# Kernel optimization log

Hardware: AMD Instinct MI355X
Metric: run time of the kernel (lower is better)

The kernel has to match this reference:

```python
import jax, jax.numpy as jnp
import numpy as np

GRID_LON = 17  # idx = lat*17 + lon in original code


def setup_inputs() -> dict:
    key = jax.random.key(0)
    ks = jax.random.split(key, 16)
    B, S, L = 512, 256, 64
    DIM_RHO, DIM_C, HID = 256, 128, 512
    N_LAT, N_LON = 17, GRID_LON

    rho = jax.random.normal(ks[0], (B, S, DIM_RHO), dtype=jnp.float32)
    c = jax.random.normal(ks[1], (1, DIM_C, N_LAT, N_LON), dtype=jnp.float32)
    w = jax.random.uniform(ks[2], (B, S), dtype=jnp.float32, minval=1e-3, maxval=1.0)
    l = jax.random.uniform(ks[3], (B,), dtype=jnp.float32, minval=0.1, maxval=10.0)
    roads = jax.random.randint(ks[4], (B, L), 0, N_LAT * N_LON)
    lon_idx = jax.random.randint(ks[5], (B, L), 0, N_LON)
    lat_idx = jax.random.randint(ks[6], (B, L), 0, N_LAT)

    sc = lambda fan_in: 1.0 / np.sqrt(fan_in)
    # f2: MLP(128, 256, 128) with selu
    f2_W1 = jax.random.uniform(ks[7], (DIM_C, 256), jnp.float32, -sc(DIM_C), sc(DIM_C))
    f2_b1 = jnp.zeros((256,), jnp.float32)
    f2_W2 = jax.random.uniform(ks[8], (256, DIM_C), jnp.float32, -sc(256), sc(256))
    f2_b2 = jnp.zeros((DIM_C,), jnp.float32)
    # f: MLP2(dim_rho + dim_c, hidden, 1) with selu (use_selu=True)
    fin = DIM_RHO + DIM_C
    f_W1 = jax.random.uniform(ks[9], (fin, HID), jnp.float32, -sc(fin), sc(fin))
    f_b1 = jnp.zeros((HID,), jnp.float32)
    f_W21 = jax.random.uniform(ks[10], (HID, 1), jnp.float32, -sc(HID), sc(HID))
    f_b21 = jnp.zeros((1,), jnp.float32)
    f_W22 = jax.random.uniform(ks[11], (HID, 1), jnp.float32, -sc(HID), sc(HID))
    f_b22 = jnp.zeros((1,), jnp.float32)

    return dict(rho=rho, c=c, w=w, l=l, roads=roads, lon_idx=lon_idx,
                lat_idx=lat_idx, f2_W1=f2_W1, f2_b1=f2_b1, f2_W2=f2_W2,
                f2_b2=f2_b2, f_W1=f_W1, f_b1=f_b1, f_W21=f_W21, f_b21=f_b21,
                f_W22=f_W22, f_b22=f_b22)


def reference(rho, c, w, l, roads, lon_idx, lat_idx,
              f2_W1, f2_b1, f2_W2, f2_b2,
              f_W1, f_b1, f_W21, f_b21, f_W22, f_b22):
    # c: (1, dim_c, n_lat, n_lon) -> (n_lat*n_lon, dim_c)
    c3 = jnp.squeeze(c, 0)                       # (dim_c, n_lat, n_lon)
    c_flat = jnp.transpose(c3, (1, 2, 0)).reshape(-1, c3.shape[0])  # (cells, dim_c)

    # ragged gather-mean, vectorized: (B, L) cell indices -> (B, dim_c)
    idx = lat_idx * GRID_LON + lon_idx           # (B, L)
    c_traj = jnp.mean(c_flat[idx], axis=1)       # (B, dim_c)

    # f2: selu MLP (dropout inactive / eval mode)
    h = jax.nn.selu(c_traj @ f2_W1 + f2_b1)
    c_tr = h @ f2_W2 + f2_b2                     # (B, dim_c)

    # broadcast over seq and concat with rho
    S = rho.shape[1]
    c_exp = jnp.broadcast_to(c_tr[:, None, :], (rho.shape[0], S, c_tr.shape[-1]))
    x = jnp.concatenate([rho, c_exp], axis=2)    # (B, S, dim_rho + dim_c)

    # f (MLP2, selu since use_selu=True)
    h1 = jax.nn.selu(x @ f_W1 + f_b1)            # (B, S, hidden)
    logm = (h1 @ f_W21 + f_b21)[..., 0]          # (B, S)
    logv = (h1 @ f_W22 + f_b22)[..., 0]          # (B, S)

    logw = jnp.log(w)
    logm_agg = jax.nn.logsumexp(logm + logw, axis=1)       # (B,)
    logv_agg = jax.nn.logsumexp(logv + 2.0 * logw, axis=1) # (B,)
    logl = jnp.log(l)
    log_mu = logl - logm_agg
    log_lambda = logl - 3.0 * logm_agg - logv_agg
    return (log_mu, log_lambda)
```

## Files before the change

### kernel.cpp

```cpp
#include <hip/hip_runtime.h>
#include <hip/hip_bf16.h>

typedef short bf16x8 __attribute__((ext_vector_type(8)));
typedef float f32x4 __attribute__((ext_vector_type(4)));
typedef _Float16 half4 __attribute__((ext_vector_type(4)));

__device__ __forceinline__ short f2bf(float f) {
    union { float f; unsigned u; } v; v.f = f;
    unsigned r = (v.u + 0x7FFFu + ((v.u >> 16) & 1u)) >> 16;
    return (short)r;
}

__device__ __forceinline__ float selu_f(float x) {
    const float scale = 1.0507009873554805f;
    const float sa = 1.0507009873554805f * 1.6732632423543772f;
    return x > 0.f ? scale * x : sa * (__expf(x) - 1.f);
}

__global__ void __launch_bounds__(512) prep_cbias_kernel(
    const float* __restrict__ c, const int* __restrict__ lat_idx,
    const int* __restrict__ lon_idx,
    const float* __restrict__ f2W1, const float* __restrict__ f2b1,
    const float* __restrict__ f2W2, const float* __restrict__ f2b2,
    const float* __restrict__ fW1, const float* __restrict__ fb1,
    float* __restrict__ cbias)
{
    __shared__ int cells[64];
    __shared__ float ctraj[128];
    __shared__ float hbuf[256];
    __shared__ float ctrf[128];
    const int b = blockIdx.x;
    const int t = threadIdx.x;

    if (t < 64) cells[t] = lat_idx[b * 64 + t] * 17 + lon_idx[b * 64 + t];
    __syncthreads();

    if (t < 128) {
        float s = 0.f;
        #pragma unroll 8
        for (int j = 0; j < 64; ++j) s += c[t * 289 + cells[j]];
        ctraj[t] = s * (1.f / 64.f);
    }
    __syncthreads();

    if (t < 256) {
        float acc = f2b1[t];
        #pragma unroll 8
        for (int i = 0; i < 128; ++i) acc += ctraj[i] * f2W1[i * 256 + t];
        hbuf[t] = selu_f(acc);
    }
    __syncthreads();

    if (t < 128) {
        float acc = f2b2[t];
        #pragma unroll 8
        for (int i = 0; i < 256; ++i) acc += hbuf[i] * f2W2[i * 128 + t];
        ctrf[t] = acc;
    }
    __syncthreads();

    float acc = fb1[t];
    #pragma unroll 8
    for (int i = 0; i < 128; ++i) acc += ctrf[i] * fW1[(256 + i) * 512 + t];
    cbias[b * 512 + t] = acc;
}

__global__ void __launch_bounds__(256) build_w1img_kernel(
    const float* __restrict__ fW1, short* __restrict__ img)
{
    int I = blockIdx.x * 256 + threadIdx.x;
    int e = I & 7;
    int lane = (I >> 3) & 63;
    int cg = (I >> 9) & 31;
    int kc = I >> 14;
    int col = cg * 16 + (lane & 15);
    int k = kc * 32 + ((lane >> 4) << 3) + e;
    img[I] = f2bf(fW1[k * 512 + col]);
}

__global__ void __launch_bounds__(256) build_wvec_kernel(
    const float* __restrict__ fW21, const float* __restrict__ fW22,
    _Float16* __restrict__ wvec)
{
    int I = blockIdx.x * 256 + threadIdx.x;
    int e = I & 3;
    int lane = (I >> 2) & 63;
    int nc = I >> 8;
    int l15 = lane & 15, hi = lane >> 4;
    int n = nc * 16 + hi * 4 + e;
    float v = (l15 == 0) ? fW21[n] : (l15 == 1 ? fW22[n] : 0.f);
    wvec[I] = (_Float16)v;
}

__global__ void __launch_bounds__(512, 4) fused_gemm_kernel(
    const float* __restrict__ rho, const short* __restrict__ w1img,
    const float* __restrict__ cbias, const _Float16* __restrict__ wvec,
    float* __restrict__ plm, float* __restrict__ plv)
{
    __shared__ __align__(16) char smA[32768];
    __shared__ float redM[8][64];
    __shared__ float redV[8][64];

    const int tid  = threadIdx.x;
    const int lane = tid & 63;
    const int w    = tid >> 6;
    const int l15  = lane & 15;
    const int hi   = lane >> 4;

    const int b   = blockIdx.x >> 2;
    const int s0v = (blockIdx.x & 3) << 6;

    {
        const float* rbase = rho + (size_t)(b * 256 + s0v) * 256;
        #pragma unroll
        for (int i = 0; i < 4; ++i) {
            int slot = i * 512 + tid;
            int kc = slot >> 8;
            int rem = slot & 255;
            int rg = rem >> 6;
            int ls = rem & 63;
            int row = rg * 16 + (ls & 15);
            int k0 = kc * 32 + ((ls >> 4) << 3);
            const float* src = rbase + (size_t)row * 256 + k0;
            float4 f0 = *(const float4*)(src);
            float4 f1 = *(const float4*)(src + 4);
            bf16x8 h;
            h[0] = f2bf(f0.x); h[1] = f2bf(f0.y); h[2] = f2bf(f0.z); h[3] = f2bf(f0.w);
            h[4] = f2bf(f1.x); h[5] = f2bf(f1.y); h[6] = f2bf(f1.z); h[7] = f2bf(f1.w);
            *(bf16x8*)(smA + slot * 16) = h;
        }
    }
    __syncthreads();

    f32x4 acc[4][4];
    #pragma unroll
    for (int nf = 0; nf < 4; ++nf)
        #pragma unroll
        for (int sf = 0; sf < 4; ++sf)
            acc[nf][sf] = (f32x4){0.f, 0.f, 0.f, 0.f};

    const char* bp = (const char*)w1img + w * 4096 + lane * 16;

    bf16x8 bN[4];
    #pragma unroll
    for (int nf = 0; nf < 4; ++nf)
        bN[nf] = *(const bf16x8*)(bp + nf * 1024);

    #pragma unroll
    for (int kc = 0; kc < 8; ++kc) {
        bf16x8 bC[4];
        #pragma unroll
        for (int nf = 0; nf < 4; ++nf) bC[nf] = bN[nf];
        if (kc < 7) {
            #pragma unroll
            for (int nf = 0; nf < 4; ++nf)
                bN[nf] = *(const bf16x8*)(bp + (size_t)(kc + 1) * 32768 + nf * 1024);
        }
        bf16x8 aF[4];
        #pragma unroll
        for (int sf = 0; sf < 4; ++sf)
            aF[sf] = *(const bf16x8*)(smA + ((kc * 4 + sf) * 64 + lane) * 16);
        #pragma unroll
        for (int nf = 0; nf < 4; ++nf)
            #pragma unroll
            for (int sf = 0; sf < 4; ++sf)
                acc[nf][sf] = __builtin_amdgcn_mfma_f32_16x16x32_bf16(
                    bC[nf], aF[sf], acc[nf][sf], 0, 0, 0);
    }

    f32x4 rd[4];
    #pragma unroll
    for (int sf = 0; sf < 4; ++sf) rd[sf] = (f32x4){0.f, 0.f, 0.f, 0.f};

    const int wn = w * 64;
    #pragma unroll
    for (int nf = 0; nf < 4; ++nf) {
        f32x4 cbf = *(const f32x4*)(cbias + b * 512 + wn + nf * 16 + hi * 4);
        half4 wv = *(const half4*)(wvec + (size_t)(w * 4 + nf) * 256 + lane * 4);
        #pragma unroll
        for (int sf = 0; sf < 4; ++sf) {
            half4 pa;
            #pragma unroll
            for (int q = 0; q < 4; ++q)
                pa[q] = (_Float16)selu_f(acc[nf][sf][q] + cbf[q]);
            rd[sf] = __builtin_amdgcn_mfma_f32_16x16x16f16(pa, wv, rd[sf], 0, 0, 0);
        }
    }

    if (l15 == 0) {
        #pragma unroll
        for (int sf = 0; sf < 4; ++sf)
            *(f32x4*)&redM[w][sf * 16 + hi * 4] = rd[sf];
    } else if (l15 == 1) {
        #pragma unroll
        for (int sf = 0; sf < 4; ++sf)
            *(f32x4*)&redV[w][sf * 16 + hi * 4] = rd[sf];
    }

    __syncthreads();
    size_t obase = (size_t)b * 256 + s0v;
    if (tid < 64) {
        float s = 0.f;
        #pragma unroll
        for (int j = 0; j < 8; ++j) s += redM[j][tid];
        plm[obase + tid] = s;
    } else if (tid < 128) {
        int rr = tid - 64;
        float s = 0.f;
        #pragma unroll
        for (int j = 0; j < 8; ++j) s += redV[j][rr];
        plv[obase + rr] = s;
    }
}

__global__ void __launch_bounds__(64) finalize_kernel(
    const float* __restrict__ plm, const float* __restrict__ plv,
    const float* __restrict__ w, const float* __restrict__ l,
    const float* __restrict__ b21p, const float* __restrict__ b22p,
    float* __restrict__ out)
{
    const int b = blockIdx.x;
    const int lane = threadIdx.x;
    const float b21 = b21p[0], b22 = b22p[0];

    float a1[4], a2[4];
    float m1 = -1e30f, m2 = -1e30f;
    #pragma unroll
    for (int i = 0; i < 4; ++i) {
        int s = i * 64 + lane;
        float lw = logf(w[b * 256 + s]);
        a1[i] = plm[b * 256 + s] + b21 + lw;
        a2[i] = plv[b * 256 + s] + b22 + 2.f * lw;
        m1 = fmaxf(m1, a1[i]);
        m2 = fmaxf(m2, a2[i]);
    }
    #pragma unroll
    for (int m = 1; m < 64; m <<= 1) {
        m1 = fmaxf(m1, __shfl_xor(m1, m));
        m2 = fmaxf(m2, __shfl_xor(m2, m));
    }
    float s1 = 0.f, s2 = 0.f;
    #pragma unroll
    for (int i = 0; i < 4; ++i) {
        s1 += expf(a1[i] - m1);
        s2 += expf(a2[i] - m2);
    }
    #pragma unroll
    for (int m = 1; m < 64; m <<= 1) {
        s1 += __shfl_xor(s1, m);
        s2 += __shfl_xor(s2, m);
    }
    if (lane == 0) {
        float lm_agg = m1 + logf(s1);
        float lv_agg = m2 + logf(s2);
        float logl = logf(l[b]);
        out[b]       = logl - lm_agg;
        out[512 + b] = logl - 3.f * lm_agg - lv_agg;
    }
}

extern "C" void kernel_launch(void* const* d_in, const int* in_sizes, int n_in,
                              void* d_out, int out_size, void* d_ws, size_t ws_size,
                              hipStream_t stream) {
    const float* rho     = (const float*)d_in[0];
    const float* c       = (const float*)d_in[1];
    const float* w       = (const float*)d_in[2];
    const float* l       = (const float*)d_in[3];
    const int*   lon_idx = (const int*)d_in[5];
    const int*   lat_idx = (const int*)d_in[6];
    const float* f2W1    = (const float*)d_in[7];
    const float* f2b1    = (const float*)d_in[8];
    const float* f2W2    = (const float*)d_in[9];
    const float* f2b2    = (const float*)d_in[10];
    const float* fW1     = (const float*)d_in[11];
    const float* fb1     = (const float*)d_in[12];
    const float* fW21    = (const float*)d_in[13];
    const float* fb21    = (const float*)d_in[14];
    const float* fW22    = (const float*)d_in[15];
    const float* fb22    = (const float*)d_in[16];
    float* out = (float*)d_out;

    char* ws = (char*)d_ws;
    float*     cbias = (float*)(ws);
    short*     w1img = (short*)(ws + 1048576);
    float*     plm   = (float*)(ws + 1310720);
    float*     plv   = (float*)(ws + 1835008);
    _Float16*  wvec  = (_Float16*)(ws + 2359296);

    prep_cbias_kernel<<<512, 512, 0, stream>>>(c, lat_idx, lon_idx,
                                               f2W1, f2b1, f2W2, f2b2,
                                               fW1, fb1, cbias);
    build_w1img_kernel<<<512, 256, 0, stream>>>(fW1, w1img);
    build_wvec_kernel<<<32, 256, 0, stream>>>(fW21, fW22, wvec);
    fused_gemm_kernel<<<2048, 512, 0, stream>>>(rho, w1img, cbias, wvec,
                                                plm, plv);
    finalize_kernel<<<512, 64, 0, stream>>>(plm, plv, w, l, fb21, fb22, out);
}
```

Measured before the change: 98.43 us.

## Merge prep kernels and pipeline GEMM with triple-buffered LDS async loads

The three preprocessing kernels become one launch that dispatches on block index. The main GEMM moves to 1024-thread blocks covering 128 sequence rows, with a 2x8 wave grid. Weight tiles are streamed into LDS through global_load_lds, and rho chunks are converted to bf16 in a triple-buffered K loop with barriers. This aims to overlap global loads with MFMA work, cut redundant per-wave weight fetches from global memory, and save launch overhead. In exchange it uses 128KB of LDS per block, which limits occupancy, and adds two barriers per K chunk.

```diff
diff --git a/kernel.cpp b/kernel.cpp
--- a/kernel.cpp
+++ b/kernel.cpp
@@ -2,6 +2,7 @@
 #include <hip/hip_bf16.h>
 
 typedef short bf16x8 __attribute__((ext_vector_type(8)));
+typedef short bf16x4 __attribute__((ext_vector_type(4)));
 typedef float f32x4 __attribute__((ext_vector_type(4)));
 typedef _Float16 half4 __attribute__((ext_vector_type(4)));
 
@@ -17,120 +18,110 @@
     return x > 0.f ? scale * x : sa * (__expf(x) - 1.f);
 }
 
-__global__ void __launch_bounds__(512) prep_cbias_kernel(
+__device__ __forceinline__ void gld_lds16(const char* g, char* l) {
+    __builtin_amdgcn_global_load_lds(
+        (const __attribute__((address_space(1))) unsigned int*)g,
+        (__attribute__((address_space(3))) unsigned int*)l, 16, 0, 0);
+}
+
+__global__ void __launch_bounds__(512) prep_all_kernel(
     const float* __restrict__ c, const int* __restrict__ lat_idx,
     const int* __restrict__ lon_idx,
     const float* __restrict__ f2W1, const float* __restrict__ f2b1,
     const float* __restrict__ f2W2, const float* __restrict__ f2b2,
     const float* __restrict__ fW1, const float* __restrict__ fb1,
+    const float* __restrict__ fW21, const float* __restrict__ fW22,
+    short* __restrict__ w1img, _Float16* __restrict__ wvec,
     float* __restrict__ cbias)
 {
-    __shared__ int cells[64];
-    __shared__ float ctraj[128];
-    __shared__ float hbuf[256];
-    __shared__ float ctrf[128];
-    const int b = blockIdx.x;
+    const int bid = blockIdx.x;
     const int t = threadIdx.x;
 
-    if (t < 64) cells[t] = lat_idx[b * 64 + t] * 17 + lon_idx[b * 64 + t];
-    __syncthreads();
-
-    if (t < 128) {
-        float s = 0.f;
+    if (bid < 512) {
+        __shared__ int cells[64];
+        __shared__ float ctraj[128];
+        __shared__ float hbuf[256];
+        __shared__ float ctrf[128];
+        const int b = bid;
+
+        if (t < 64) cells[t] = lat_idx[b * 64 + t] * 17 + lon_idx[b * 64 + t];
+        __syncthreads();
+
+        if (t < 128) {
+            float s = 0.f;
+            #pragma unroll 8
+            for (int j = 0; j < 64; ++j) s += c[t * 289 + cells[j]];
+            ctraj[t] = s * (1.f / 64.f);
+        }
+        __syncthreads();
+
+        if (t < 256) {
+            float acc = f2b1[t];
+            #pragma unroll 8
+            for (int i = 0; i < 128; ++i) acc += ctraj[i] * f2W1[i * 256 + t];
+            hbuf[t] = selu_f(acc);
+        }
+        __syncthreads();
+
+        if (t < 128) {
+            float acc = f2b2[t];
+            #pragma unroll 8
+            for (int i = 0; i < 256; ++i) acc += hbuf[i] * f2W2[i * 128 + t];
+            ctrf[t] = acc;
+        }
+        __syncthreads();
+
+        float acc = fb1[t];
         #pragma unroll 8
-        for (int j = 0; j < 64; ++j) s += c[t * 289 + cells[j]];
-        ctraj[t] = s * (1.f / 64.f);
-    }
-    __syncthreads();
-
-    if (t < 256) {
-        float acc = f2b1[t];
-        #pragma unroll 8
-        for (int i = 0; i < 128; ++i) acc += ctraj[i] * f2W1[i * 256 + t];
-        hbuf[t] = selu_f(acc);
-    }
-    __syncthreads();
-
-    if (t < 128) {
-        float acc = f2b2[t];
-        #pragma unroll 8
-        for (int i = 0; i < 256; ++i) acc += hbuf[i] * f2W2[i * 128 + t];
-        ctrf[t] = acc;
-    }
-    __syncthreads();
-
-    float acc = fb1[t];
-    #pragma unroll 8
-    for (int i = 0; i < 128; ++i) acc += ctrf[i] * fW1[(256 + i) * 512 + t];
-    cbias[b * 512 + t] = acc;
-}
-
-__global__ void __launch_bounds__(256) build_w1img_kernel(
-    const float* __restrict__ fW1, short* __restrict__ img)
-{
-    int I = blockIdx.x * 256 + threadIdx.x;
-    int e = I & 7;
-    int lane = (I >> 3) & 63;
-    int cg = (I >> 9) & 31;
-    int kc = I >> 14;
-    int col = cg * 16 + (lane & 15);
-    int k = kc * 32 + ((lane >> 4) << 3) + e;
-    img[I] = f2bf(fW1[k * 512 + col]);
-}
-
-__global__ void __launch_bounds__(256) build_wvec_kernel(
-    const float* __restrict__ fW21, const float* __restrict__ fW22,
-    _Float16* __restrict__ wvec)
-{
-    int I = blockIdx.x * 256 + threadIdx.x;
-    int e = I & 3;
-    int lane = (I >> 2) & 63;
-    int nc = I >> 8;
-    int l15 = lane & 15, hi = lane >> 4;
-    int n = nc * 16 + hi * 4 + e;
-    float v = (l15 == 0) ? fW21[n] : (l15 == 1 ? fW22[n] : 0.f);
-    wvec[I] = (_Float16)v;
-}
-
-__global__ void __launch_bounds__(512, 4) fused_gemm_kernel(
+        for (int i = 0; i < 128; ++i) acc += ctrf[i] * fW1[(256 + i) * 512 + t];
+        cbias[b * 512 + t] = acc;
+    } else if (bid < 768) {
+        int I = (bid - 512) * 512 + t;
+        int e = I & 7;
+        int lane = (I >> 3) & 63;
+        int cg = (I >> 9) & 31;
+        int kc = I >> 14;
+        int col = cg * 16 + (lane & 15);
+        int k = kc * 32 + ((lane >> 4) << 3) + e;
+        w1img[I] = f2bf(fW1[k * 512 + col]);
+    } else {
+        int I = (bid - 768) * 512 + t;
+        int e = I & 3;
+        int lane = (I >> 2) & 63;
+        int nc = I >> 8;
+        int l15 = lane & 15, hi = lane >> 4;
+        int n = nc * 16 + hi * 4 + e;
+        float v = (l15 == 0) ? fW21[n] : (l15 == 1 ? fW22[n] : 0.f);
+        wvec[I] = (_Float16)v;
+    }
+}
+
+__global__ void __launch_bounds__(1024, 4) fused_gemm_kernel(
     const float* __restrict__ rho, const short* __restrict__ w1img,
     const float* __restrict__ cbias, const _Float16* __restrict__ wvec,
     float* __restrict__ plm, float* __restrict__ plv)
 {
-    __shared__ __align__(16) char smA[32768];
-    __shared__ float redM[8][64];
-    __shared__ float redV[8][64];
+    __shared__ __align__(16) char smem[131072];
 
     const int tid  = threadIdx.x;
     const int lane = tid & 63;
-    const int w    = tid >> 6;
+    const int wid  = tid >> 6;
+    const int wr   = wid >> 3;
+    const int wc2  = wid & 7;
     const int l15  = lane & 15;
     const int hi   = lane >> 4;
 
-    const int b   = blockIdx.x >> 2;
-    const int s0v = (blockIdx.x & 3) << 6;
-
-    {
-        const float* rbase = rho + (size_t)(b * 256 + s0v) * 256;
-        #pragma unroll
-        for (int i = 0; i < 4; ++i) {
-            int slot = i * 512 + tid;
-            int kc = slot >> 8;
-            int rem = slot & 255;
-            int rg = rem >> 6;
-            int ls = rem & 63;
-            int row = rg * 16 + (ls & 15);
-            int k0 = kc * 32 + ((ls >> 4) << 3);
-            const float* src = rbase + (size_t)row * 256 + k0;
-            float4 f0 = *(const float4*)(src);
-            float4 f1 = *(const float4*)(src + 4);
-            bf16x8 h;
-            h[0] = f2bf(f0.x); h[1] = f2bf(f0.y); h[2] = f2bf(f0.z); h[3] = f2bf(f0.w);
-            h[4] = f2bf(f1.x); h[5] = f2bf(f1.y); h[6] = f2bf(f1.z); h[7] = f2bf(f1.w);
-            *(bf16x8*)(smA + slot * 16) = h;
-        }
-    }
-    __syncthreads();
+    const int b  = blockIdx.x >> 1;
+    const int s0 = (blockIdx.x & 1) << 7;
+
+    const int rg_t = tid >> 7;
+    const int ln_t = (tid >> 1) & 63;
+    const int h_t  = tid & 1;
+    const float* prA = rho + (size_t)(b * 256 + s0 + rg_t * 16 + (ln_t & 15)) * 256
+                           + ((ln_t >> 4) << 3) + h_t * 4;
+    const int awoff = ((rg_t * 64 + ln_t) << 4) + (h_t << 3);
+
+    const char* wsrc = (const char*)w1img;
 
     f32x4 acc[4][4];
     #pragma unroll
@@ -139,44 +130,79 @@
         for (int sf = 0; sf < 4; ++sf)
             acc[nf][sf] = (f32x4){0.f, 0.f, 0.f, 0.f};
 
-    const char* bp = (const char*)w1img + w * 4096 + lane * 16;
-
-    bf16x8 bN[4];
-    #pragma unroll
-    for (int nf = 0; nf < 4; ++nf)
-        bN[nf] = *(const bf16x8*)(bp + nf * 1024);
-
-    #pragma unroll
-    for (int kc = 0; kc < 8; ++kc) {
-        bf16x8 bC[4];
-        #pragma unroll
-        for (int nf = 0; nf < 4; ++nf) bC[nf] = bN[nf];
-        if (kc < 7) {
-            #pragma unroll
-            for (int nf = 0; nf < 4; ++nf)
-                bN[nf] = *(const bf16x8*)(bp + (size_t)(kc + 1) * 32768 + nf * 1024);
-        }
-        bf16x8 aF[4];
-        #pragma unroll
-        for (int sf = 0; sf < 4; ++sf)
-            aF[sf] = *(const bf16x8*)(smA + ((kc * 4 + sf) * 64 + lane) * 16);
-        #pragma unroll
-        for (int nf = 0; nf < 4; ++nf)
-            #pragma unroll
-            for (int sf = 0; sf < 4; ++sf)
-                acc[nf][sf] = __builtin_amdgcn_mfma_f32_16x16x32_bf16(
-                    bC[nf], aF[sf], acc[nf][sf], 0, 0, 0);
-    }
+    float4 pf0, pf1;
+
+    {
+        const char* bs0 = wsrc + (wid * 2) * 1024 + lane * 16;
+        char* bd0 = smem + 24576 + (wid * 2) * 1024;
+        gld_lds16(bs0, bd0);
+        gld_lds16(bs0 + 1024, bd0 + 1024);
+        pf0 = *(const float4*)(prA);
+        const char* bs1 = wsrc + 32768 + (wid * 2) * 1024 + lane * 16;
+        char* bd1 = smem + 24576 + 32768 + (wid * 2) * 1024;
+        gld_lds16(bs1, bd1);
+        gld_lds16(bs1 + 1024, bd1 + 1024);
+        pf1 = *(const float4*)(prA + 8);
+    }
+
+#define CHUNK(I, PFX)                                                          \
+    {                                                                          \
+        {          \
+          bf16x4 hh;                                                           \
+          hh[0] = f2bf(PFX.x); hh[1] = f2bf(PFX.y);                            \
+          hh[2] = f2bf(PFX.z); hh[3] = f2bf(PFX.w);                            \
+          *(bf16x4*)(smem + ((I) % 3) * 8192 + awoff) = hh; }                  \
+        if ((I) + 2 <= 7) {    \
+            const char* bs = wsrc + ((I) + 2) * 32768 + (wid * 2) * 1024       \
+                             + lane * 16;                                      \
+            char* bd = smem + 24576 + (((I) + 2) % 3) * 32768                  \
+                       + (wid * 2) * 1024;                                     \
+            gld_lds16(bs, bd);                                                 \
+            gld_lds16(bs + 1024, bd + 1024);                                   \
+            PFX = *(const float4*)(prA + ((I) + 2) * 8);                       \
+        }                                                                      \
+        asm volatile("s_waitcnt lgkmcnt(0)" ::: "memory");                     \
+        __builtin_amdgcn_s_barrier();                                          \
+        __builtin_amdgcn_sched_barrier(0);                                     \
+        {                                                                      \
+            bf16x8 aF[4], bF[4];                                               \
+            const char* ab = smem + ((I) % 3) * 8192;                          \
+            const char* bb = smem + 24576 + ((I) % 3) * 32768;                 \
+            _Pragma("unroll")                                                  \
+            for (int sf = 0; sf < 4; ++sf)                                     \
+                aF[sf] = *(const bf16x8*)(ab + (((wr * 4 + sf) * 64 + lane) << 4)); \
+            _Pragma("unroll")                                                  \
+            for (int nf = 0; nf < 4; ++nf)                                     \
+                bF[nf] = *(const bf16x8*)(bb + (((wc2 * 4 + nf) * 64 + lane) << 4)); \
+            _Pragma("unroll")                                                  \
+            for (int nf = 0; nf < 4; ++nf)                                     \
+                _Pragma("unroll")                                              \
+                for (int sf = 0; sf < 4; ++sf)                                 \
+                    acc[nf][sf] = __builtin_amdgcn_mfma_f32_16x16x32_bf16(     \
+                        bF[nf], aF[sf], acc[nf][sf], 0, 0, 0);                 \
+        }                                                                      \
+        __builtin_amdgcn_sched_barrier(0);                                     \
+        __builtin_amdgcn_s_barrier();                                          \
+    }
+
+    CHUNK(0, pf0)
+    CHUNK(1, pf1)
+    CHUNK(2, pf0)
+    CHUNK(3, pf1)
+    CHUNK(4, pf0)
+    CHUNK(5, pf1)
+    CHUNK(6, pf0)
+    CHUNK(7, pf1)
+#undef CHUNK
 
     f32x4 rd[4];
     #pragma unroll
     for (int sf = 0; sf < 4; ++sf) rd[sf] = (f32x4){0.f, 0.f, 0.f, 0.f};
 
-    const int wn = w * 64;
     #pragma unroll
     for (int nf = 0; nf < 4; ++nf) {
-        f32x4 cbf = *(const f32x4*)(cbias + b * 512 + wn + nf * 16 + hi * 4);
-        half4 wv = *(const half4*)(wvec + (size_t)(w * 4 + nf) * 256 + lane * 4);
+        f32x4 cbf = *(const f32x4*)(cbias + b * 512 + wc2 * 64 + nf * 16 + hi * 4);
+        half4 wv = *(const half4*)(wvec + (size_t)(wc2 * 4 + nf) * 256 + lane * 4);
         #pragma unroll
         for (int sf = 0; sf < 4; ++sf) {
             half4 pa;
@@ -187,28 +213,30 @@
         }
     }
 
+    float* redM = (float*)(smem + 122880);
+    float* redV = (float*)(smem + 126976);
     if (l15 == 0) {
         #pragma unroll
         for (int sf = 0; sf < 4; ++sf)
-            *(f32x4*)&redM[w][sf * 16 + hi * 4] = rd[sf];
+            *(f32x4*)&redM[wc2 * 128 + wr * 64 + sf * 16 + hi * 4] = rd[sf];
     } else if (l15 == 1) {
         #pragma unroll
         for (int sf = 0; sf < 4; ++sf)
-            *(f32x4*)&redV[w][sf * 16 + hi * 4] = rd[sf];
+            *(f32x4*)&redV[wc2 * 128 + wr * 64 + sf * 16 + hi * 4] = rd[sf];
     }
 
     __syncthreads();
-    size_t obase = (size_t)b * 256 + s0v;
-    if (tid < 64) {
+    size_t obase = (size_t)b * 256 + s0;
+    if (tid < 128) {
         float s = 0.f;
         #pragma unroll
-        for (int j = 0; j < 8; ++j) s += redM[j][tid];
+        for (int j = 0; j < 8; ++j) s += redM[j * 128 + tid];
         plm[obase + tid] = s;
-    } else if (tid < 128) {
-        int rr = tid - 64;
+    } else if (tid < 256) {
+        int rr = tid - 128;
         float s = 0.f;
         #pragma unroll
-        for (int j = 0; j < 8; ++j) s += redV[j][rr];
+        for (int j = 0; j < 8; ++j) s += redV[j * 128 + rr];
         plv[obase + rr] = s;
     }
 }
@@ -287,12 +315,11 @@
     float*     plv   = (float*)(ws + 1835008);
     _Float16*  wvec  = (_Float16*)(ws + 2359296);
 
-    prep_cbias_kernel<<<512, 512, 0, stream>>>(c, lat_idx, lon_idx,
-                                               f2W1, f2b1, f2W2, f2b2,
-                                               fW1, fb1, cbias);
-    build_w1img_kernel<<<512, 256, 0, stream>>>(fW1, w1img);
-    build_wvec_kernel<<<32, 256, 0, stream>>>(fW21, fW22, wvec);
-    fused_gemm_kernel<<<2048, 512, 0, stream>>>(rho, w1img, cbias, wvec,
-                                                plm, plv);
+    prep_all_kernel<<<784, 512, 0, stream>>>(c, lat_idx, lon_idx,
+                                             f2W1, f2b1, f2W2, f2b2,
+                                             fW1, fb1, fW21, fW22,
+                                             w1img, wvec, cbias);
+    fused_gemm_kernel<<<1024, 1024, 0, stream>>>(rho, w1img, cbias, wvec,
+                                                 plm, plv);
     finalize_kernel<<<512, 64, 0, stream>>>(plm, plv, w, l, fb21, fb22, out);
 }
```

Result: no change. 99.94 us (+1.5%).

## Merge prep kernels and coalesce rho staging with swizzled LDS layout

Applied to the files above, without the earlier changes.

Folds the three small preparation kernels into one launch by giving each block range its own task, which removes two kernel launches and their gaps. In the GEMM kernel, rho is now read with contiguous per-thread loads and converted to bf16 with packed hardware conversion instructions. The result is stored into LDS with an XOR swizzle, and the MFMA operand reads use the matching swizzled addresses to avoid bank conflicts. The reduction buffers are carved out of the same shared allocation. The swizzle indexing must exactly match the old fragment layout, which is the main correctness risk.

```diff
diff --git a/kernel.cpp b/kernel.cpp
--- a/kernel.cpp
+++ b/kernel.cpp
@@ -17,79 +17,76 @@
     return x > 0.f ? scale * x : sa * (__expf(x) - 1.f);
 }
 
-__global__ void __launch_bounds__(512) prep_cbias_kernel(
+__global__ void __launch_bounds__(512) prep_all_kernel(
     const float* __restrict__ c, const int* __restrict__ lat_idx,
     const int* __restrict__ lon_idx,
     const float* __restrict__ f2W1, const float* __restrict__ f2b1,
     const float* __restrict__ f2W2, const float* __restrict__ f2b2,
     const float* __restrict__ fW1, const float* __restrict__ fb1,
+    const float* __restrict__ fW21, const float* __restrict__ fW22,
+    short* __restrict__ w1img, _Float16* __restrict__ wvec,
     float* __restrict__ cbias)
 {
-    __shared__ int cells[64];
-    __shared__ float ctraj[128];
-    __shared__ float hbuf[256];
-    __shared__ float ctrf[128];
-    const int b = blockIdx.x;
+    const int bid = blockIdx.x;
     const int t = threadIdx.x;
 
-    if (t < 64) cells[t] = lat_idx[b * 64 + t] * 17 + lon_idx[b * 64 + t];
-    __syncthreads();
-
-    if (t < 128) {
-        float s = 0.f;
+    if (bid < 512) {
+        __shared__ int cells[64];
+        __shared__ float ctraj[128];
+        __shared__ float hbuf[256];
+        __shared__ float ctrf[128];
+        const int b = bid;
+
+        if (t < 64) cells[t] = lat_idx[b * 64 + t] * 17 + lon_idx[b * 64 + t];
+        __syncthreads();
+
+        if (t < 128) {
+            float s = 0.f;
+            #pragma unroll 8
+            for (int j = 0; j < 64; ++j) s += c[t * 289 + cells[j]];
+            ctraj[t] = s * (1.f / 64.f);
+        }
+        __syncthreads();
+
+        if (t < 256) {
+            float acc = f2b1[t];
+            #pragma unroll 8
+            for (int i = 0; i < 128; ++i) acc += ctraj[i] * f2W1[i * 256 + t];
+            hbuf[t] = selu_f(acc);
+        }
+        __syncthreads();
+
+        if (t < 128) {
+            float acc = f2b2[t];
+            #pragma unroll 8
+            for (int i = 0; i < 256; ++i) acc += hbuf[i] * f2W2[i * 128 + t];
+            ctrf[t] = acc;
+        }
+        __syncthreads();
+
+        float acc = fb1[t];
         #pragma unroll 8
-        for (int j = 0; j < 64; ++j) s += c[t * 289 + cells[j]];
-        ctraj[t] = s * (1.f / 64.f);
-    }
-    __syncthreads();
-
-    if (t < 256) {
-        float acc = f2b1[t];
-        #pragma unroll 8
-        for (int i = 0; i < 128; ++i) acc += ctraj[i] * f2W1[i * 256 + t];
-        hbuf[t] = selu_f(acc);
-    }
-    __syncthreads();
-
-    if (t < 128) {
-        float acc = f2b2[t];
-        #pragma unroll 8
-        for (int i = 0; i < 256; ++i) acc += hbuf[i] * f2W2[i * 128 + t];
-        ctrf[t] = acc;
-    }
-    __syncthreads();
-
-    float acc = fb1[t];
-    #pragma unroll 8
-    for (int i = 0; i < 128; ++i) acc += ctrf[i] * fW1[(256 + i) * 512 + t];
-    cbias[b * 512 + t] = acc;
-}
-
-__global__ void __launch_bounds__(256) build_w1img_kernel(
-    const float* __restrict__ fW1, short* __restrict__ img)
-{
-    int I = blockIdx.x * 256 + threadIdx.x;
-    int e = I & 7;
-    int lane = (I >> 3) & 63;
-    int cg = (I >> 9) & 31;
-    int kc = I >> 14;
-    int col = cg * 16 + (lane & 15);
-    int k = kc * 32 + ((lane >> 4) << 3) + e;
-    img[I] = f2bf(fW1[k * 512 + col]);
-}
-
-__global__ void __launch_bounds__(256) build_wvec_kernel(
-    const float* __restrict__ fW21, const float* __restrict__ fW22,
-    _Float16* __restrict__ wvec)
-{
-    int I = blockIdx.x * 256 + threadIdx.x;
-    int e = I & 3;
-    int lane = (I >> 2) & 63;
-    int nc = I >> 8;
-    int l15 = lane & 15, hi = lane >> 4;
-    int n = nc * 16 + hi * 4 + e;
-    float v = (l15 == 0) ? fW21[n] : (l15 == 1 ? fW22[n] : 0.f);
-    wvec[I] = (_Float16)v;
+        for (int i = 0; i < 128; ++i) acc += ctrf[i] * fW1[(256 + i) * 512 + t];
+        cbias[b * 512 + t] = acc;
+    } else if (bid < 768) {
+        int I = (bid - 512) * 512 + t;
+        int e = I & 7;
+        int lane = (I >> 3) & 63;
+        int cg = (I >> 9) & 31;
+        int kc = I >> 14;
+        int col = cg * 16 + (lane & 15);
+        int k = kc * 32 + ((lane >> 4) << 3) + e;
+        w1img[I] = f2bf(fW1[k * 512 + col]);
+    } else {
+        int I = (bid - 768) * 512 + t;
+        int e = I & 3;
+        int lane = (I >> 2) & 63;
+        int nc = I >> 8;
+        int l15 = lane & 15, hi = lane >> 4;
+        int n = nc * 16 + hi * 4 + e;
+        float v = (l15 == 0) ? fW21[n] : (l15 == 1 ? fW22[n] : 0.f);
+        wvec[I] = (_Float16)v;
+    }
 }
 
 __global__ void __launch_bounds__(512, 4) fused_gemm_kernel(
@@ -97,9 +94,7 @@
     const float* __restrict__ cbias, const _Float16* __restrict__ wvec,
     float* __restrict__ plm, float* __restrict__ plv)
 {
-    __shared__ __align__(16) char smA[32768];
-    __shared__ float redM[8][64];
-    __shared__ float redV[8][64];
+    __shared__ __align__(16) char smA[36864];
 
     const int tid  = threadIdx.x;
     const int lane = tid & 63;
@@ -107,27 +102,25 @@
     const int l15  = lane & 15;
     const int hi   = lane >> 4;
 
-    const int b   = blockIdx.x >> 2;
-    const int s0v = (blockIdx.x & 3) << 6;
+    const int b  = blockIdx.x >> 2;
+    const int s0 = (blockIdx.x & 3) << 6;
 
     {
-        const float* rbase = rho + (size_t)(b * 256 + s0v) * 256;
-        #pragma unroll
-        for (int i = 0; i < 4; ++i) {
-            int slot = i * 512 + tid;
-            int kc = slot >> 8;
-            int rem = slot & 255;
-            int rg = rem >> 6;
-            int ls = rem & 63;
-            int row = rg * 16 + (ls & 15);
-            int k0 = kc * 32 + ((ls >> 4) << 3);
-            const float* src = rbase + (size_t)row * 256 + k0;
-            float4 f0 = *(const float4*)(src);
-            float4 f1 = *(const float4*)(src + 4);
-            bf16x8 h;
-            h[0] = f2bf(f0.x); h[1] = f2bf(f0.y); h[2] = f2bf(f0.z); h[3] = f2bf(f0.w);
-            h[4] = f2bf(f1.x); h[5] = f2bf(f1.y); h[6] = f2bf(f1.z); h[7] = f2bf(f1.w);
-            *(bf16x8*)(smA + slot * 16) = h;
+        const float* src = rho + (size_t)(b * 256 + s0) * 256 + tid * 8;
+        const int kc_w = (tid >> 2) & 7;
+        const int hi_w = tid & 3;
+        const int sw_w = (tid >> 5) ^ (tid & 15);
+        #pragma unroll
+        for (int j = 0; j < 4; ++j) {
+            float4 f0 = *(const float4*)(src + j * 4096);
+            float4 f1 = *(const float4*)(src + j * 4096 + 4);
+            union { bf16x8 h; unsigned u[4]; } pk;
+            asm("v_cvt_pk_bf16_f32 %0, %1, %2" : "=v"(pk.u[0]) : "v"(f0.x), "v"(f0.y));
+            asm("v_cvt_pk_bf16_f32 %0, %1, %2" : "=v"(pk.u[1]) : "v"(f0.z), "v"(f0.w));
+            asm("v_cvt_pk_bf16_f32 %0, %1, %2" : "=v"(pk.u[2]) : "v"(f1.x), "v"(f1.y));
+            asm("v_cvt_pk_bf16_f32 %0, %1, %2" : "=v"(pk.u[3]) : "v"(f1.z), "v"(f1.w));
+            int slot = (kc_w * 4 + j) * 64 + hi_w * 16 + sw_w;
+            *(bf16x8*)(smA + (slot << 4)) = pk.h;
         }
     }
     __syncthreads();
@@ -156,10 +149,12 @@
             for (int nf = 0; nf < 4; ++nf)
                 bN[nf] = *(const bf16x8*)(bp + (size_t)(kc + 1) * 32768 + nf * 1024);
         }
+        const int sw_r = l15 ^ (((kc & 3) << 2) | hi);
+        const char* ab = smA + ((kc * 256 + hi * 16 + sw_r) << 4);
         bf16x8 aF[4];
         #pragma unroll
         for (int sf = 0; sf < 4; ++sf)
-            aF[sf] = *(const bf16x8*)(smA + ((kc * 4 + sf) * 64 + lane) * 16);
+            aF[sf] = *(const bf16x8*)(ab + sf * 1024);
         #pragma unroll
         for (int nf = 0; nf < 4; ++nf)
             #pragma unroll
@@ -172,10 +167,9 @@
     #pragma unroll
     for (int sf = 0; sf < 4; ++sf) rd[sf] = (f32x4){0.f, 0.f, 0.f, 0.f};
 
-    const int wn = w * 64;
     #pragma unroll
     for (int nf = 0; nf < 4; ++nf) {
-        f32x4 cbf = *(const f32x4*)(cbias + b * 512 + wn + nf * 16 + hi * 4);
+        f32x4 cbf = *(const f32x4*)(cbias + b * 512 + w * 64 + nf * 16 + hi * 4);
         half4 wv = *(const half4*)(wvec + (size_t)(w * 4 + nf) * 256 + lane * 4);
         #pragma unroll
         for (int sf = 0; sf < 4; ++sf) {
@@ -187,28 +181,30 @@
         }
     }
 
+    float* redM = (float*)(smA + 32768);
+    float* redV = (float*)(smA + 34816);
     if (l15 == 0) {
         #pragma unroll
         for (int sf = 0; sf < 4; ++sf)
-            *(f32x4*)&redM[w][sf * 16 + hi * 4] = rd[sf];
+            *(f32x4*)&redM[w * 64 + sf * 16 + hi * 4] = rd[sf];
     } else if (l15 == 1) {
         #pragma unroll
         for (int sf = 0; sf < 4; ++sf)
-            *(f32x4*)&redV[w][sf * 16 + hi * 4] = rd[sf];
+            *(f32x4*)&redV[w * 64 + sf * 16 + hi * 4] = rd[sf];
     }
 
     __syncthreads();
-    size_t obase = (size_t)b * 256 + s0v;
+    size_t obase = (size_t)b * 256 + s0;
     if (tid < 64) {
         float s = 0.f;
         #pragma unroll
-        for (int j = 0; j < 8; ++j) s += redM[j][tid];
+        for (int j = 0; j < 8; ++j) s += redM[j * 64 + tid];
         plm[obase + tid] = s;
     } else if (tid < 128) {
         int rr = tid - 64;
         float s = 0.f;
         #pragma unroll
-        for (int j = 0; j < 8; ++j) s += redV[j][rr];
+        for (int j = 0; j < 8; ++j) s += redV[j * 64 + rr];
         plv[obase + rr] = s;
     }
 }
@@ -287,11 +283,10 @@
     float*     plv   = (float*)(ws + 1835008);
     _Float16*  wvec  = (_Float16*)(ws + 2359296);
 
-    prep_cbias_kernel<<<512, 512, 0, stream>>>(c, lat_idx, lon_idx,
-                                               f2W1, f2b1, f2W2, f2b2,
-                                               fW1, fb1, cbias);
-    build_w1img_kernel<<<512, 256, 0, stream>>>(fW1, w1img);
-    build_wvec_kernel<<<32, 256, 0, stream>>>(fW21, fW22, wvec);
+    prep_all_kernel<<<784, 512, 0, stream>>>(c, lat_idx, lon_idx,
+                                             f2W1, f2b1, f2W2, f2b2,
+                                             fW1, fb1, fW21, fW22,
+                                             w1img, wvec, cbias);
     fused_gemm_kernel<<<2048, 512, 0, stream>>>(rho, w1img, cbias, wvec,
                                                 plm, plv);
     finalize_kernel<<<512, 64, 0, stream>>>(plm, plv, w, l, fb21, fb22, out);
```

New measurement: 92.33 us, median of 3. 1.07x faster.
